# Kernel optimization log

Hardware: AMD Instinct MI355X
Metric: run time of the kernel (lower is better)

The kernel has to match this reference:

```python
import jax, jax.numpy as jnp
import numpy as np

B, S, E, H, V, L = 64, 128, 512, 1024, 32000, 1


def setup_inputs() -> dict:
    key = jax.random.key(0)
    ks = jax.random.split(key, 12)
    def rn(k, shape, scale=0.02):
        return jax.random.normal(k, shape, dtype=jnp.float32) * scale
    return dict(
        emb=rn(ks[0], (B, E), 1.0),
        hidden=rn(ks[1], (L, B, H), 1.0),
        encoder_outputs=rn(ks[2], (S, B, H), 1.0),
        z=rn(ks[3], (B, H), 1.0),
        # Attn('concat'): W_a [H, 2H], bias, scoring vector v [H]
        Wa=rn(ks[4], (H, 2 * H)), ba=jnp.zeros((H,), jnp.float32),
        v=rn(ks[5], (H,)),
        # CustomGRUCell: input/hidden/context/latent-z to 3*H gate projections
        Wx=rn(ks[6], (3 * H, E)), bx=jnp.zeros((3 * H,), jnp.float32),
        Wh=rn(ks[7], (3 * H, H)), bh=jnp.zeros((3 * H,), jnp.float32),
        Wc=rn(ks[8], (3 * H, H)), bc=jnp.zeros((3 * H,), jnp.float32),
        Wz=rn(ks[9], (3 * H, H)), bz=jnp.zeros((3 * H,), jnp.float32),
        # rnn2out: Linear(H, V)
        Wout=rn(ks[10], (V, H)), bout=jnp.zeros((V,), jnp.float32),
    )


def reference(emb, hidden, encoder_outputs, z, Wa, ba, v,
              Wx, bx, Wh, bh, Wc, bc, Wz, bz, Wout, bout):
    h_last = hidden[-1]                                              # [B,H]
    # Bahdanau 'concat' attention: score = v . tanh(Wa @ [h; enc] + ba)
    hS = jnp.broadcast_to(h_last[None], encoder_outputs.shape)       # [S,B,H]
    energy = jnp.tanh(jnp.concatenate([hS, encoder_outputs], axis=-1) @ Wa.T + ba)  # [S,B,H]
    scores = jnp.einsum('sbh,h->bs', energy, v)                      # [B,S]
    attn_weights = jax.nn.softmax(scores, axis=-1)[:, None, :]       # [B,1,S]
    enc_bt = jnp.transpose(encoder_outputs, (1, 0, 2))               # [B,S,H]
    context = jnp.einsum('bos,bsh->bh', attn_weights, enc_bt)        # [B,H]
    # Custom GRU cell: gates get extra context and latent-z additive terms
    gx = emb @ Wx.T + bx                                             # [B,3H]
    gh = h_last @ Wh.T + bh
    gc = context @ Wc.T + bc
    gz = z @ Wz.T + bz
    xr, xu, xn = jnp.split(gx + gc + gz, 3, axis=-1)
    hr, hu, hn = jnp.split(gh, 3, axis=-1)
    r = jax.nn.sigmoid(xr + hr)                                      # reset gate
    u = jax.nn.sigmoid(xu + hu)                                      # update gate
    n = jnp.tanh(xn + r * hn)                                        # candidate
    h_new = (1.0 - u) * n + u * h_last                               # [B,H]
    out = h_new @ Wout.T + bout                                      # [B,V] logits
    return out, h_new[None], attn_weights
```

## Files before the change

### kernel.cpp

```cpp
#include <hip/hip_runtime.h>
#include <hip/hip_bf16.h>
#include <math.h>

#define B_  64
#define S_  128
#define E_  512
#define H_  1024
#define V_  32000
#define H3_ 3072
#define NT_ 16

typedef __attribute__((ext_vector_type(8))) short bf16x8;
typedef __attribute__((ext_vector_type(4))) float f32x4;

__device__ __forceinline__ unsigned short f2b(float f) {
    unsigned int u = __builtin_bit_cast(unsigned int, f);
    u = (u + 0x7fffu + ((u >> 16) & 1u)) >> 16;
    return (unsigned short)u;
}

__device__ __forceinline__ void tile_acc(const float* __restrict__ A, int lda,
                                         const float* __restrict__ Wrow0, int ldw,
                                         int kspan, int t, float c[4][4],
                                         float (*As)[64], float (*Ws)[64]) {
    const int tx = t & 15, ty = t >> 4;
    const int lm = t >> 2;
    const int lk = (t & 3) * 4;
    for (int k0 = 0; k0 < kspan; k0 += 16) {
        float4 av = *(const float4*)&A[lm * lda + k0 + lk];
        float4 wv = *(const float4*)&Wrow0[(size_t)lm * ldw + k0 + lk];
        As[lk + 0][lm] = av.x; As[lk + 1][lm] = av.y;
        As[lk + 2][lm] = av.z; As[lk + 3][lm] = av.w;
        Ws[lk + 0][lm] = wv.x; Ws[lk + 1][lm] = wv.y;
        Ws[lk + 2][lm] = wv.z; Ws[lk + 3][lm] = wv.w;
        __syncthreads();
        #pragma unroll
        for (int k = 0; k < 16; ++k) {
            float4 a = *(const float4*)&As[k][ty * 4];
            float4 w = *(const float4*)&Ws[k][tx * 4];
            c[0][0] += a.x * w.x; c[0][1] += a.x * w.y; c[0][2] += a.x * w.z; c[0][3] += a.x * w.w;
            c[1][0] += a.y * w.x; c[1][1] += a.y * w.y; c[1][2] += a.y * w.z; c[1][3] += a.y * w.w;
            c[2][0] += a.z * w.x; c[2][1] += a.z * w.y; c[2][2] += a.z * w.z; c[2][3] += a.z * w.w;
            c[3][0] += a.w * w.x; c[3][1] += a.w * w.y; c[3][2] += a.w * w.z; c[3][3] += a.w * w.w;
        }
        __syncthreads();
    }
}

__device__ __forceinline__ void hproj_body(int bx, int by, const float* __restrict__ h,
                                           const float* __restrict__ Wa, float* __restrict__ hpp,
                                           int t, float (*As)[64], float (*Ws)[64]) {
    const int n0 = bx * 64;
    const int kb = by * 128;
    const int tx = t & 15, ty = t >> 4;
    float c[4][4];
    #pragma unroll
    for (int i = 0; i < 4; ++i)
        #pragma unroll
        for (int j = 0; j < 4; ++j) c[i][j] = 0.f;
    tile_acc(&h[kb], H_, &Wa[(size_t)n0 * (2 * H_) + kb], 2 * H_, 128, t, c, As, Ws);
    float* dst = hpp + (size_t)by * B_ * H_;
    #pragma unroll
    for (int i = 0; i < 4; ++i) {
        const int m = ty * 4 + i;
        #pragma unroll
        for (int j = 0; j < 4; ++j)
            dst[m * H_ + n0 + tx * 4 + j] = c[i][j];
    }
}

__global__ __launch_bounds__(256) void prologue(
    const float* __restrict__ enc, const float* __restrict__ Wa,
    const float* __restrict__ h, unsigned short* __restrict__ encb,
    unsigned short* __restrict__ wa2b, float* __restrict__ hpp) {
    __shared__ float As[16][64];
    __shared__ float Ws[16][64];
    const int bid = blockIdx.x;
    const int t = threadIdx.x;
    if (bid < 4096) {
        const size_t i8 = ((size_t)bid * 256 + t) * 8;
        float4 a = *(const float4*)&enc[i8];
        float4 b = *(const float4*)&enc[i8 + 4];
        unsigned short o[8] = { f2b(a.x), f2b(a.y), f2b(a.z), f2b(a.w),
                                f2b(b.x), f2b(b.y), f2b(b.z), f2b(b.w) };
        *(uint4*)&encb[i8] = *(uint4*)o;
    } else if (bid < 4608) {
        const int id = (bid - 4096) * 256 + t;
        const int n = id >> 7;
        const int kk = (id & 127) * 8;
        const float* src = &Wa[(size_t)n * (2 * H_) + H_ + kk];
        float4 a = *(const float4*)src;
        float4 b = *(const float4*)(src + 4);
        unsigned short o[8] = { f2b(a.x), f2b(a.y), f2b(a.z), f2b(a.w),
                                f2b(b.x), f2b(b.y), f2b(b.z), f2b(b.w) };
        *(uint4*)&wa2b[(size_t)n * H_ + kk] = *(uint4*)o;
    } else {
        const int id = bid - 4608;
        hproj_body(id & 15, id >> 4, h, Wa, hpp, t, As, Ws);
    }
}

__global__ void hproj_splitk(const float* __restrict__ h, const float* __restrict__ Wa,
                             float* __restrict__ hpp) {
    __shared__ float As[16][64];
    __shared__ float Ws[16][64];
    hproj_body(blockIdx.x, blockIdx.y, h, Wa, hpp, threadIdx.x, As, Ws);
}

__global__ void reduce_hproj(const float* __restrict__ hpp, const float* __restrict__ ba,
                             float* __restrict__ hproj) {
    const int idx = blockIdx.x * 256 + threadIdx.x;
    const int hh = idx & 1023;
    float s = ba[hh];
    #pragma unroll
    for (int c = 0; c < 8; ++c) s += hpp[(size_t)c * B_ * H_ + idx];
    hproj[idx] = s;
}

__global__ __launch_bounds__(256) void energy_mfma(
    const unsigned short* __restrict__ Ab, const unsigned short* __restrict__ Bb,
    const float* __restrict__ hproj, const float* __restrict__ v,
    float* __restrict__ partials) {
    __shared__ unsigned short As[128 * 32];
    __shared__ unsigned short Bs[128 * 32];
    const int nb = blockIdx.x;
    const int mb = blockIdx.y;
    const int m0 = mb * 128, n0 = nb * 128;
    const int t = threadIdx.x;
    const int lane = t & 63, w = t >> 6;
    const int wr = w >> 1, wc = w & 1;

    f32x4 acc[4][4];
    #pragma unroll
    for (int i = 0; i < 4; ++i)
        #pragma unroll
        for (int j = 0; j < 4; ++j) acc[i][j] = (f32x4){0.f, 0.f, 0.f, 0.f};

    for (int k0 = 0; k0 < H_; k0 += 32) {
        #pragma unroll
        for (int r = 0; r < 2; ++r) {
            const int c = r * 256 + t;
            const int row = c >> 2, slot = c & 3;
            const int sw = slot ^ ((row >> 1) & 3);
            uint4 da = *(const uint4*)&Ab[(size_t)(m0 + row) * H_ + k0 + slot * 8];
            *(uint4*)((char*)As + row * 64 + sw * 16) = da;
            uint4 db = *(const uint4*)&Bb[(size_t)(n0 + row) * H_ + k0 + slot * 8];
            *(uint4*)((char*)Bs + row * 64 + sw * 16) = db;
        }
        __syncthreads();
        bf16x8 a[4], b[4];
        #pragma unroll
        for (int i = 0; i < 4; ++i) {
            const int row = wr * 64 + i * 16 + (lane & 15);
            const int sw = (lane >> 4) ^ ((row >> 1) & 3);
            a[i] = *(const bf16x8*)((const char*)As + row * 64 + sw * 16);
        }
        #pragma unroll
        for (int j = 0; j < 4; ++j) {
            const int row = wc * 64 + j * 16 + (lane & 15);
            const int sw = (lane >> 4) ^ ((row >> 1) & 3);
            b[j] = *(const bf16x8*)((const char*)Bs + row * 64 + sw * 16);
        }
        #pragma unroll
        for (int i = 0; i < 4; ++i)
            #pragma unroll
            for (int j = 0; j < 4; ++j)
                acc[i][j] = __builtin_amdgcn_mfma_f32_16x16x32_bf16(a[i], b[j], acc[i][j], 0, 0, 0);
        __syncthreads();
    }

    float vj[4];
    #pragma unroll
    for (int j = 0; j < 4; ++j) vj[j] = v[n0 + wc * 64 + j * 16 + (lane & 15)];

    const int s = mb * 2 + wr;
    #pragma unroll
    for (int i = 0; i < 4; ++i) {
        #pragma unroll
        for (int q = 0; q < 4; ++q) {
            const int b = i * 16 + (lane >> 4) * 4 + q;
            float sum = 0.f;
            #pragma unroll
            for (int j = 0; j < 4; ++j) {
                const int n = n0 + wc * 64 + j * 16 + (lane & 15);
                sum += vj[j] * tanhf(acc[i][j][q] + hproj[b * H_ + n]);
            }
            sum += __shfl_xor(sum, 1);
            sum += __shfl_xor(sum, 2);
            sum += __shfl_xor(sum, 4);
            sum += __shfl_xor(sum, 8);
            if ((lane & 15) == 0)
                partials[((size_t)b * S_ + s) * NT_ + nb * 2 + wc] = sum;
        }
    }
}

__global__ void energy_scores(const float* __restrict__ enc, const float* __restrict__ Wa,
                              const float* __restrict__ hproj, const float* __restrict__ v,
                              float* __restrict__ partials) {
    __shared__ float As[16][64];
    __shared__ float Ws[16][64];
    __shared__ float red[64][16];
    const int nt = blockIdx.x;
    const int s  = blockIdx.y;
    const int n0 = nt * 64;
    const float* Arow = enc + (size_t)s * (B_ * H_);
    const int t  = threadIdx.x;
    const int tx = t & 15, ty = t >> 4;
    float c[4][4];
    #pragma unroll
    for (int i = 0; i < 4; ++i)
        #pragma unroll
        for (int j = 0; j < 4; ++j) c[i][j] = 0.f;
    tile_acc(Arow, H_, &Wa[(size_t)n0 * (2 * H_) + H_], 2 * H_, H_, t, c, As, Ws);
    #pragma unroll
    for (int i = 0; i < 4; ++i) {
        const int b = ty * 4 + i;
        float part = 0.f;
        #pragma unroll
        for (int j = 0; j < 4; ++j) {
            const int h = n0 + tx * 4 + j;
            part += v[h] * tanhf(c[i][j] + hproj[b * H_ + h]);
        }
        red[b][tx] = part;
    }
    __syncthreads();
    if (t < 64) {
        float sum = 0.f;
        #pragma unroll
        for (int x = 0; x < 16; ++x) sum += red[t][x];
        partials[((size_t)t * S_ + s) * NT_ + nt] = sum;
    }
}

__global__ __launch_bounds__(256) void softmax_ctx(
    const float* __restrict__ spart, const float* __restrict__ enc,
    float* __restrict__ attn, float* __restrict__ ctx) {
    __shared__ float red[128];
    __shared__ float aw[128];
    const int b = blockIdx.y;
    const int t = threadIdx.x;
    if (t < 128) {
        float sc = 0.f;
        #pragma unroll
        for (int nt = 0; nt < NT_; ++nt) sc += spart[((size_t)b * S_ + t) * NT_ + nt];
        aw[t] = sc;
        red[t] = sc;
    }
    __syncthreads();
    for (int o = 64; o > 0; o >>= 1) {
        if (t < o) red[t] = fmaxf(red[t], red[t + o]);
        __syncthreads();
    }
    const float mx = red[0];
    __syncthreads();
    if (t < 128) { aw[t] = expf(aw[t] - mx); red[t] = aw[t]; }
    __syncthreads();
    for (int o = 64; o > 0; o >>= 1) {
        if (t < o) red[t] += red[t + o];
        __syncthreads();
    }
    const float inv = 1.f / red[0];
    if (t < 128) {
        aw[t] *= inv;
        if (blockIdx.x == 0) attn[b * S_ + t] = aw[t];
    }
    __syncthreads();
    const int h = blockIdx.x * 256 + t;
    float acc = 0.f;
    for (int s = 0; s < S_; ++s)
        acc += aw[s] * enc[((size_t)s * B_ + b) * H_ + h];
    ctx[b * H_ + h] = acc;
}

__global__ void gates_splitk(const float* __restrict__ emb, const float* __restrict__ z,
                             const float* __restrict__ ctx, const float* __restrict__ h,
                             const float* __restrict__ Wx, const float* __restrict__ Wz,
                             const float* __restrict__ Wc, const float* __restrict__ Wh,
                             float* __restrict__ P) {
    __shared__ float As[16][64];
    __shared__ float Ws[16][64];
    const int n0 = blockIdx.x * 64;
    const int yc = blockIdx.y;
    const int t  = threadIdx.x;
    const int tx = t & 15, ty = t >> 4;

    const float* A; const float* W; int lda, kb;
    if (yc == 0)      { A = emb; W = Wx; lda = E_; kb = 0; }
    else if (yc <= 2) { A = z;   W = Wz; lda = H_; kb = (yc - 1) * 512; }
    else if (yc <= 4) { A = ctx; W = Wc; lda = H_; kb = (yc - 3) * 512; }
    else              { A = h;   W = Wh; lda = H_; kb = (yc - 5) * 512; }

    float c[4][4];
    #pragma unroll
    for (int i = 0; i < 4; ++i)
        #pragma unroll
        for (int j = 0; j < 4; ++j) c[i][j] = 0.f;
    tile_acc(&A[kb], lda, &W[(size_t)n0 * lda + kb], lda, 512, t, c, As, Ws);
    float* dst = P + (size_t)yc * B_ * H3_;
    #pragma unroll
    for (int i = 0; i < 4; ++i) {
        const int m = ty * 4 + i;
        #pragma unroll
        for (int j = 0; j < 4; ++j)
            dst[m * H3_ + n0 + tx * 4 + j] = c[i][j];
    }
}

__global__ void gru_k(const float* __restrict__ P, const float* __restrict__ hlast,
                      const float* __restrict__ bx, const float* __restrict__ bz,
                      const float* __restrict__ bc, const float* __restrict__ bh,
                      float* __restrict__ hnew, unsigned short* __restrict__ hnewb) {
    const int idx = blockIdx.x * 256 + threadIdx.x;
    const int b = idx >> 10, h = idx & 1023;
    float x[3], hg[3];
    #pragma unroll
    for (int g = 0; g < 3; ++g) {
        const int col = g * H_ + h;
        float sx = bx[col] + bz[col] + bc[col];
        #pragma unroll
        for (int c = 0; c < 5; ++c) sx += P[((size_t)c * B_ + b) * H3_ + col];
        float sh = bh[col];
        #pragma unroll
        for (int c = 5; c < 7; ++c) sh += P[((size_t)c * B_ + b) * H3_ + col];
        x[g] = sx; hg[g] = sh;
    }
    const float r = 1.f / (1.f + expf(-(x[0] + hg[0])));
    const float u = 1.f / (1.f + expf(-(x[1] + hg[1])));
    const float n = tanhf(x[2] + r * hg[2]);
    const float val = (1.f - u) * n + u * hlast[idx];
    hnew[idx] = val;
    if (hnewb) hnewb[idx] = f2b(val);
}

__global__ __launch_bounds__(256) void wout_mfma(
    const unsigned short* __restrict__ Ab, const float* __restrict__ W,
    const float* __restrict__ bias, float* __restrict__ C) {
    __shared__ unsigned short As[64 * 64];
    __shared__ unsigned short Bs[64 * 64];
    const int n0 = blockIdx.x * 64;
    const int t = threadIdx.x;
    const int lane = t & 63, w = t >> 6;
    const int wr = w >> 1, wc = w & 1;

    f32x4 acc[2][2];
    #pragma unroll
    for (int i = 0; i < 2; ++i)
        #pragma unroll
        for (int j = 0; j < 2; ++j) acc[i][j] = (f32x4){0.f, 0.f, 0.f, 0.f};

    for (int k0 = 0; k0 < H_; k0 += 64) {
        #pragma unroll
        for (int r = 0; r < 2; ++r) {
            const int c = r * 256 + t;
            const int row = c >> 3, slot = c & 7;
            const int sw = slot ^ (row & 7);
            uint4 da = *(const uint4*)&Ab[(size_t)row * H_ + k0 + slot * 8];
            *(uint4*)((char*)As + row * 128 + sw * 16) = da;
        }
        #pragma unroll
        for (int r = 0; r < 4; ++r) {
            const int c = r * 256 + t;
            const int row = c >> 4, q4 = c & 15;
            const float4 wv = *(const float4*)&W[(size_t)(n0 + row) * H_ + k0 + q4 * 4];
            uint2 pk;
            pk.x = (unsigned int)f2b(wv.x) | ((unsigned int)f2b(wv.y) << 16);
            pk.y = (unsigned int)f2b(wv.z) | ((unsigned int)f2b(wv.w) << 16);
            const int slot = q4 >> 1, half = q4 & 1;
            const int sw = slot ^ (row & 7);
            *(uint2*)((char*)Bs + row * 128 + sw * 16 + half * 8) = pk;
        }
        __syncthreads();
        #pragma unroll
        for (int kk = 0; kk < 2; ++kk) {
            bf16x8 a[2], b[2];
            #pragma unroll
            for (int i = 0; i < 2; ++i) {
                const int row = wr * 32 + i * 16 + (lane & 15);
                const int sw = (kk * 4 + (lane >> 4)) ^ (row & 7);
                a[i] = *(const bf16x8*)((const char*)As + row * 128 + sw * 16);
            }
            #pragma unroll
            for (int j = 0; j < 2; ++j) {
                const int row = wc * 32 + j * 16 + (lane & 15);
                const int sw = (kk * 4 + (lane >> 4)) ^ (row & 7);
                b[j] = *(const bf16x8*)((const char*)Bs + row * 128 + sw * 16);
            }
            #pragma unroll
            for (int i = 0; i < 2; ++i)
                #pragma unroll
                for (int j = 0; j < 2; ++j)
                    acc[i][j] = __builtin_amdgcn_mfma_f32_16x16x32_bf16(a[i], b[j], acc[i][j], 0, 0, 0);
        }
        __syncthreads();
    }

    #pragma unroll
    for (int i = 0; i < 2; ++i)
        #pragma unroll
        for (int j = 0; j < 2; ++j) {
            const int n = n0 + wc * 32 + j * 16 + (lane & 15);
            const float bn = bias[n];
            #pragma unroll
            for (int q = 0; q < 4; ++q) {
                const int m = wr * 32 + i * 16 + (lane >> 4) * 4 + q;
                C[(size_t)m * V_ + n] = acc[i][j][q] + bn;
            }
        }
}

__global__ void gemm_nt(const float* __restrict__ A, const float* __restrict__ W,
                        const float* __restrict__ bias, float* __restrict__ C,
                        int N, int K) {
    __shared__ float As[16][64];
    __shared__ float Ws[16][64];
    const int n0 = blockIdx.x * 64;
    const int t  = threadIdx.x;
    const int tx = t & 15, ty = t >> 4;
    float c[4][4];
    #pragma unroll
    for (int i = 0; i < 4; ++i)
        #pragma unroll
        for (int j = 0; j < 4; ++j) c[i][j] = 0.f;
    tile_acc(A, K, &W[(size_t)n0 * K], K, K, t, c, As, Ws);
    #pragma unroll
    for (int i = 0; i < 4; ++i) {
        const int m = ty * 4 + i;
        #pragma unroll
        for (int j = 0; j < 4; ++j) {
            const int n = n0 + tx * 4 + j;
            C[m * N + n] = c[i][j] + bias[n];
        }
    }
}

extern "C" void kernel_launch(void* const* d_in, const int* in_sizes, int n_in,
                              void* d_out, int out_size, void* d_ws, size_t ws_size,
                              hipStream_t stream) {
    const float* emb   = (const float*)d_in[0];
    const float* hid   = (const float*)d_in[1];
    const float* enc   = (const float*)d_in[2];
    const float* z     = (const float*)d_in[3];
    const float* Wa    = (const float*)d_in[4];
    const float* ba    = (const float*)d_in[5];
    const float* v     = (const float*)d_in[6];
    const float* Wx    = (const float*)d_in[7];
    const float* bx    = (const float*)d_in[8];
    const float* Wh    = (const float*)d_in[9];
    const float* bh    = (const float*)d_in[10];
    const float* Wc    = (const float*)d_in[11];
    const float* bc    = (const float*)d_in[12];
    const float* Wz    = (const float*)d_in[13];
    const float* bz    = (const float*)d_in[14];
    const float* Wout  = (const float*)d_in[15];
    const float* bout  = (const float*)d_in[16];

    float* out  = (float*)d_out;
    float* hnew = out + (size_t)B_ * V_;
    float* attn = hnew + (size_t)B_ * H_;

    float* hproj = (float*)d_ws;
    float* spart = hproj + (size_t)B_ * H_;
    float* ctx   = spart + (size_t)B_ * S_ * NT_;
    float* hpp   = ctx + (size_t)B_ * H_;
    float* uni   = hpp + (size_t)8 * B_ * H_;
    unsigned short* encb = (unsigned short*)uni;
    unsigned short* wa2b = encb + (size_t)S_ * B_ * H_;
    float* P = uni;
    unsigned short* hnewb = (unsigned short*)(P + (size_t)7 * B_ * H3_);
    const size_t need = (size_t)((char*)(wa2b + (size_t)H_ * H_) - (char*)d_ws);

    const float* hlast = hid;
    dim3 blk(256);

    const bool fast = (ws_size >= need);
    if (fast) {
        prologue<<<dim3(4736), blk, 0, stream>>>(enc, Wa, hlast, encb, wa2b, hpp);
        reduce_hproj<<<dim3((B_ * H_) / 256), blk, 0, stream>>>(hpp, ba, hproj);
        energy_mfma<<<dim3(H_ / 128, (S_ * B_) / 128), blk, 0, stream>>>(encb, wa2b, hproj, v, spart);
    } else {
        hproj_splitk<<<dim3(H_ / 64, 8), blk, 0, stream>>>(hlast, Wa, hpp);
        reduce_hproj<<<dim3((B_ * H_) / 256), blk, 0, stream>>>(hpp, ba, hproj);
        energy_scores<<<dim3(NT_, S_), blk, 0, stream>>>(enc, Wa, hproj, v, spart);
    }

    softmax_ctx<<<dim3(H_ / 256, B_), blk, 0, stream>>>(spart, enc, attn, ctx);

    gates_splitk<<<dim3(H3_ / 64, 7), blk, 0, stream>>>(emb, z, ctx, hlast,
                                                        Wx, Wz, Wc, Wh, P);
    gru_k<<<dim3((B_ * H_) / 256), blk, 0, stream>>>(P, hlast, bx, bz, bc, bh,
                                                     hnew, fast ? hnewb : nullptr);

    if (fast) {
        wout_mfma<<<dim3(V_ / 64), blk, 0, stream>>>(hnewb, Wout, bout, out);
    } else {
        gemm_nt<<<dim3(V_ / 64), blk, 0, stream>>>(hnew, Wout, bout, out, V_, H_);
    }
}
```

Baseline: 142.0 us.

## Fold context-independent gate GEMMs into prologue and widen energy K-tile to 64

The emb, z and h gate projections do not depend on the attention context, so they now run as extra blocks of the prologue kernel. Only the two context split-K chunks remain in a separate gates_ctx launch after softmax. This takes work off the serial critical path and lets it overlap with the bf16 conversion blocks. The energy MFMA kernel also doubles its K step to 64 with an 8-slot XOR swizzle, halving the number of barriers per tile at the cost of more shared memory. The workspace is re-laid out so P no longer aliases encb and wa2b, which raises the workspace requirement.

```diff
diff --git a/kernel.cpp b/kernel.cpp
--- a/kernel.cpp
+++ b/kernel.cpp
@@ -69,10 +69,43 @@
     }
 }
 
+__device__ __forceinline__ void gate_body(int n0, int sel,
+                                          const float* __restrict__ emb, const float* __restrict__ z,
+                                          const float* __restrict__ h,
+                                          const float* __restrict__ Wx, const float* __restrict__ Wz,
+                                          const float* __restrict__ Wh, float* __restrict__ P,
+                                          int t, float (*As)[64], float (*Ws)[64]) {
+    const int tx = t & 15, ty = t >> 4;
+    const float* A; const float* W; int lda, kb, chunk;
+    if (sel == 0)      { A = emb; W = Wx; lda = E_; kb = 0;   chunk = 0; }
+    else if (sel == 1) { A = z;   W = Wz; lda = H_; kb = 0;   chunk = 1; }
+    else if (sel == 2) { A = z;   W = Wz; lda = H_; kb = 512; chunk = 2; }
+    else if (sel == 3) { A = h;   W = Wh; lda = H_; kb = 0;   chunk = 5; }
+    else               { A = h;   W = Wh; lda = H_; kb = 512; chunk = 6; }
+    float c[4][4];
+    #pragma unroll
+    for (int i = 0; i < 4; ++i)
+        #pragma unroll
+        for (int j = 0; j < 4; ++j) c[i][j] = 0.f;
+    tile_acc(&A[kb], lda, &W[(size_t)n0 * lda + kb], lda, 512, t, c, As, Ws);
+    float* dst = P + (size_t)chunk * B_ * H3_;
+    #pragma unroll
+    for (int i = 0; i < 4; ++i) {
+        const int m = ty * 4 + i;
+        #pragma unroll
+        for (int j = 0; j < 4; ++j)
+            dst[m * H3_ + n0 + tx * 4 + j] = c[i][j];
+    }
+}
+
 __global__ __launch_bounds__(256) void prologue(
     const float* __restrict__ enc, const float* __restrict__ Wa,
-    const float* __restrict__ h, unsigned short* __restrict__ encb,
-    unsigned short* __restrict__ wa2b, float* __restrict__ hpp) {
+    const float* __restrict__ h, const float* __restrict__ emb,
+    const float* __restrict__ z,
+    const float* __restrict__ Wx, const float* __restrict__ Wz,
+    const float* __restrict__ Wh,
+    unsigned short* __restrict__ encb, unsigned short* __restrict__ wa2b,
+    float* __restrict__ hpp, float* __restrict__ P) {
     __shared__ float As[16][64];
     __shared__ float Ws[16][64];
     const int bid = blockIdx.x;
@@ -94,9 +127,12 @@
         unsigned short o[8] = { f2b(a.x), f2b(a.y), f2b(a.z), f2b(a.w),
                                 f2b(b.x), f2b(b.y), f2b(b.z), f2b(b.w) };
         *(uint4*)&wa2b[(size_t)n * H_ + kk] = *(uint4*)o;
-    } else {
+    } else if (bid < 4736) {
         const int id = bid - 4608;
         hproj_body(id & 15, id >> 4, h, Wa, hpp, t, As, Ws);
+    } else {
+        const int id = bid - 4736;
+        gate_body((id % 48) * 64, id / 48, emb, z, h, Wx, Wz, Wh, P, t, As, Ws);
     }
 }
 
@@ -121,8 +157,8 @@
     const unsigned short* __restrict__ Ab, const unsigned short* __restrict__ Bb,
     const float* __restrict__ hproj, const float* __restrict__ v,
     float* __restrict__ partials) {
-    __shared__ unsigned short As[128 * 32];
-    __shared__ unsigned short Bs[128 * 32];
+    __shared__ unsigned short As[128 * 64];
+    __shared__ unsigned short Bs[128 * 64];
     const int nb = blockIdx.x;
     const int mb = blockIdx.y;
     const int m0 = mb * 128, n0 = nb * 128;
@@ -136,36 +172,39 @@
         #pragma unroll
         for (int j = 0; j < 4; ++j) acc[i][j] = (f32x4){0.f, 0.f, 0.f, 0.f};
 
-    for (int k0 = 0; k0 < H_; k0 += 32) {
-        #pragma unroll
-        for (int r = 0; r < 2; ++r) {
+    for (int k0 = 0; k0 < H_; k0 += 64) {
+        #pragma unroll
+        for (int r = 0; r < 4; ++r) {
             const int c = r * 256 + t;
-            const int row = c >> 2, slot = c & 3;
-            const int sw = slot ^ ((row >> 1) & 3);
+            const int row = c >> 3, slot = c & 7;
+            const int sw = slot ^ (row & 7);
             uint4 da = *(const uint4*)&Ab[(size_t)(m0 + row) * H_ + k0 + slot * 8];
-            *(uint4*)((char*)As + row * 64 + sw * 16) = da;
+            *(uint4*)((char*)As + row * 128 + sw * 16) = da;
             uint4 db = *(const uint4*)&Bb[(size_t)(n0 + row) * H_ + k0 + slot * 8];
-            *(uint4*)((char*)Bs + row * 64 + sw * 16) = db;
-        }
-        __syncthreads();
-        bf16x8 a[4], b[4];
-        #pragma unroll
-        for (int i = 0; i < 4; ++i) {
-            const int row = wr * 64 + i * 16 + (lane & 15);
-            const int sw = (lane >> 4) ^ ((row >> 1) & 3);
-            a[i] = *(const bf16x8*)((const char*)As + row * 64 + sw * 16);
-        }
-        #pragma unroll
-        for (int j = 0; j < 4; ++j) {
-            const int row = wc * 64 + j * 16 + (lane & 15);
-            const int sw = (lane >> 4) ^ ((row >> 1) & 3);
-            b[j] = *(const bf16x8*)((const char*)Bs + row * 64 + sw * 16);
-        }
-        #pragma unroll
-        for (int i = 0; i < 4; ++i)
-            #pragma unroll
-            for (int j = 0; j < 4; ++j)
-                acc[i][j] = __builtin_amdgcn_mfma_f32_16x16x32_bf16(a[i], b[j], acc[i][j], 0, 0, 0);
+            *(uint4*)((char*)Bs + row * 128 + sw * 16) = db;
+        }
+        __syncthreads();
+        #pragma unroll
+        for (int kk = 0; kk < 2; ++kk) {
+            bf16x8 a[4], b[4];
+            #pragma unroll
+            for (int i = 0; i < 4; ++i) {
+                const int row = wr * 64 + i * 16 + (lane & 15);
+                const int sw = (kk * 4 + (lane >> 4)) ^ (row & 7);
+                a[i] = *(const bf16x8*)((const char*)As + row * 128 + sw * 16);
+            }
+            #pragma unroll
+            for (int j = 0; j < 4; ++j) {
+                const int row = wc * 64 + j * 16 + (lane & 15);
+                const int sw = (kk * 4 + (lane >> 4)) ^ (row & 7);
+                b[j] = *(const bf16x8*)((const char*)Bs + row * 128 + sw * 16);
+            }
+            #pragma unroll
+            for (int i = 0; i < 4; ++i)
+                #pragma unroll
+                for (int j = 0; j < 4; ++j)
+                    acc[i][j] = __builtin_amdgcn_mfma_f32_16x16x32_bf16(a[i], b[j], acc[i][j], 0, 0, 0);
+        }
         __syncthreads();
     }
 
@@ -273,6 +312,30 @@
     ctx[b * H_ + h] = acc;
 }
 
+__global__ void gates_ctx(const float* __restrict__ ctx, const float* __restrict__ Wc,
+                          float* __restrict__ P) {
+    __shared__ float As[16][64];
+    __shared__ float Ws[16][64];
+    const int n0 = blockIdx.x * 64;
+    const int kb = blockIdx.y * 512;
+    const int t  = threadIdx.x;
+    const int tx = t & 15, ty = t >> 4;
+    float c[4][4];
+    #pragma unroll
+    for (int i = 0; i < 4; ++i)
+        #pragma unroll
+        for (int j = 0; j < 4; ++j) c[i][j] = 0.f;
+    tile_acc(&ctx[kb], H_, &Wc[(size_t)n0 * H_ + kb], H_, 512, t, c, As, Ws);
+    float* dst = P + (size_t)(3 + blockIdx.y) * B_ * H3_;
+    #pragma unroll
+    for (int i = 0; i < 4; ++i) {
+        const int m = ty * 4 + i;
+        #pragma unroll
+        for (int j = 0; j < 4; ++j)
+            dst[m * H3_ + n0 + tx * 4 + j] = c[i][j];
+    }
+}
+
 __global__ void gates_splitk(const float* __restrict__ emb, const float* __restrict__ z,
                              const float* __restrict__ ctx, const float* __restrict__ h,
                              const float* __restrict__ Wx, const float* __restrict__ Wz,
@@ -284,13 +347,11 @@
     const int yc = blockIdx.y;
     const int t  = threadIdx.x;
     const int tx = t & 15, ty = t >> 4;
-
     const float* A; const float* W; int lda, kb;
     if (yc == 0)      { A = emb; W = Wx; lda = E_; kb = 0; }
     else if (yc <= 2) { A = z;   W = Wz; lda = H_; kb = (yc - 1) * 512; }
     else if (yc <= 4) { A = ctx; W = Wc; lda = H_; kb = (yc - 3) * 512; }
     else              { A = h;   W = Wh; lda = H_; kb = (yc - 5) * 512; }
-
     float c[4][4];
     #pragma unroll
     for (int i = 0; i < 4; ++i)
@@ -463,11 +524,11 @@
     float* spart = hproj + (size_t)B_ * H_;
     float* ctx   = spart + (size_t)B_ * S_ * NT_;
     float* hpp   = ctx + (size_t)B_ * H_;
-    float* uni   = hpp + (size_t)8 * B_ * H_;
-    unsigned short* encb = (unsigned short*)uni;
-    unsigned short* wa2b = encb + (size_t)S_ * B_ * H_;
-    float* P = uni;
-    unsigned short* hnewb = (unsigned short*)(P + (size_t)7 * B_ * H3_);
+    float* P     = hpp + (size_t)8 * B_ * H_;
+    float* fend  = P + (size_t)7 * B_ * H3_;
+    unsigned short* hnewb = (unsigned short*)fend;
+    unsigned short* encb  = hnewb + (size_t)B_ * H_;
+    unsigned short* wa2b  = encb + (size_t)S_ * B_ * H_;
     const size_t need = (size_t)((char*)(wa2b + (size_t)H_ * H_) - (char*)d_ws);
 
     const float* hlast = hid;
@@ -475,25 +536,22 @@
 
     const bool fast = (ws_size >= need);
     if (fast) {
-        prologue<<<dim3(4736), blk, 0, stream>>>(enc, Wa, hlast, encb, wa2b, hpp);
+        prologue<<<dim3(4976), blk, 0, stream>>>(enc, Wa, hlast, emb, z,
+                                                 Wx, Wz, Wh, encb, wa2b, hpp, P);
         reduce_hproj<<<dim3((B_ * H_) / 256), blk, 0, stream>>>(hpp, ba, hproj);
         energy_mfma<<<dim3(H_ / 128, (S_ * B_) / 128), blk, 0, stream>>>(encb, wa2b, hproj, v, spart);
+        softmax_ctx<<<dim3(H_ / 256, B_), blk, 0, stream>>>(spart, enc, attn, ctx);
+        gates_ctx<<<dim3(H3_ / 64, 2), blk, 0, stream>>>(ctx, Wc, P);
+        gru_k<<<dim3((B_ * H_) / 256), blk, 0, stream>>>(P, hlast, bx, bz, bc, bh, hnew, hnewb);
+        wout_mfma<<<dim3(V_ / 64), blk, 0, stream>>>(hnewb, Wout, bout, out);
     } else {
         hproj_splitk<<<dim3(H_ / 64, 8), blk, 0, stream>>>(hlast, Wa, hpp);
         reduce_hproj<<<dim3((B_ * H_) / 256), blk, 0, stream>>>(hpp, ba, hproj);
         energy_scores<<<dim3(NT_, S_), blk, 0, stream>>>(enc, Wa, hproj, v, spart);
-    }
-
-    softmax_ctx<<<dim3(H_ / 256, B_), blk, 0, stream>>>(spart, enc, attn, ctx);
-
-    gates_splitk<<<dim3(H3_ / 64, 7), blk, 0, stream>>>(emb, z, ctx, hlast,
-                                                        Wx, Wz, Wc, Wh, P);
-    gru_k<<<dim3((B_ * H_) / 256), blk, 0, stream>>>(P, hlast, bx, bz, bc, bh,
-                                                     hnew, fast ? hnewb : nullptr);
-
-    if (fast) {
-        wout_mfma<<<dim3(V_ / 64), blk, 0, stream>>>(hnewb, Wout, bout, out);
-    } else {
+        softmax_ctx<<<dim3(H_ / 256, B_), blk, 0, stream>>>(spart, enc, attn, ctx);
+        gates_splitk<<<dim3(H3_ / 64, 7), blk, 0, stream>>>(emb, z, ctx, hlast,
+                                                            Wx, Wz, Wc, Wh, P);
+        gru_k<<<dim3((B_ * H_) / 256), blk, 0, stream>>>(P, hlast, bx, bz, bc, bh, hnew, nullptr);
         gemm_nt<<<dim3(V_ / 64), blk, 0, stream>>>(hnew, Wout, bout, out, V_, H_);
     }
 }
```

Result: slower. 178.8 us (+25.9%).

## Deepen split-K for gates, prefetch tile loads, widen energy MFMA K-step

Applied to the files above, without the earlier changes.

The gates GEMM now splits K into 256-wide chunks across 14 blocks in y instead of 7, so more blocks run in parallel. gru_k sums the extra partials. tile_acc prefetches the next global tile into registers while computing on the current shared-memory tile, which hides load latency. energy_mfma now stages a K-slab of 64 with an 8-way XOR swizzle, halving barriers per K. The workspace layout is reordered so the larger partial buffer and the bf16 buffers do not overlap, at the cost of more workspace and more partial-sum traffic.

```diff
diff --git a/kernel.cpp b/kernel.cpp
--- a/kernel.cpp
+++ b/kernel.cpp
@@ -9,6 +9,7 @@
 #define V_  32000
 #define H3_ 3072
 #define NT_ 16
+#define NGC 14
 
 typedef __attribute__((ext_vector_type(8))) short bf16x8;
 typedef __attribute__((ext_vector_type(4))) float f32x4;
@@ -26,14 +27,18 @@
     const int tx = t & 15, ty = t >> 4;
     const int lm = t >> 2;
     const int lk = (t & 3) * 4;
+    float4 av = *(const float4*)&A[lm * lda + lk];
+    float4 wv = *(const float4*)&Wrow0[(size_t)lm * ldw + lk];
     for (int k0 = 0; k0 < kspan; k0 += 16) {
-        float4 av = *(const float4*)&A[lm * lda + k0 + lk];
-        float4 wv = *(const float4*)&Wrow0[(size_t)lm * ldw + k0 + lk];
         As[lk + 0][lm] = av.x; As[lk + 1][lm] = av.y;
         As[lk + 2][lm] = av.z; As[lk + 3][lm] = av.w;
         Ws[lk + 0][lm] = wv.x; Ws[lk + 1][lm] = wv.y;
         Ws[lk + 2][lm] = wv.z; Ws[lk + 3][lm] = wv.w;
         __syncthreads();
+        if (k0 + 16 < kspan) {
+            av = *(const float4*)&A[lm * lda + k0 + 16 + lk];
+            wv = *(const float4*)&Wrow0[(size_t)lm * ldw + k0 + 16 + lk];
+        }
         #pragma unroll
         for (int k = 0; k < 16; ++k) {
             float4 a = *(const float4*)&As[k][ty * 4];
@@ -121,8 +126,8 @@
     const unsigned short* __restrict__ Ab, const unsigned short* __restrict__ Bb,
     const float* __restrict__ hproj, const float* __restrict__ v,
     float* __restrict__ partials) {
-    __shared__ unsigned short As[128 * 32];
-    __shared__ unsigned short Bs[128 * 32];
+    __shared__ unsigned short As[128 * 64];
+    __shared__ unsigned short Bs[128 * 64];
     const int nb = blockIdx.x;
     const int mb = blockIdx.y;
     const int m0 = mb * 128, n0 = nb * 128;
@@ -136,36 +141,39 @@
         #pragma unroll
         for (int j = 0; j < 4; ++j) acc[i][j] = (f32x4){0.f, 0.f, 0.f, 0.f};
 
-    for (int k0 = 0; k0 < H_; k0 += 32) {
-        #pragma unroll
-        for (int r = 0; r < 2; ++r) {
+    for (int k0 = 0; k0 < H_; k0 += 64) {
+        #pragma unroll
+        for (int r = 0; r < 4; ++r) {
             const int c = r * 256 + t;
-            const int row = c >> 2, slot = c & 3;
-            const int sw = slot ^ ((row >> 1) & 3);
+            const int row = c >> 3, slot = c & 7;
+            const int sw = slot ^ (row & 7);
             uint4 da = *(const uint4*)&Ab[(size_t)(m0 + row) * H_ + k0 + slot * 8];
-            *(uint4*)((char*)As + row * 64 + sw * 16) = da;
+            *(uint4*)((char*)As + row * 128 + sw * 16) = da;
             uint4 db = *(const uint4*)&Bb[(size_t)(n0 + row) * H_ + k0 + slot * 8];
-            *(uint4*)((char*)Bs + row * 64 + sw * 16) = db;
-        }
-        __syncthreads();
-        bf16x8 a[4], b[4];
-        #pragma unroll
-        for (int i = 0; i < 4; ++i) {
-            const int row = wr * 64 + i * 16 + (lane & 15);
-            const int sw = (lane >> 4) ^ ((row >> 1) & 3);
-            a[i] = *(const bf16x8*)((const char*)As + row * 64 + sw * 16);
-        }
-        #pragma unroll
-        for (int j = 0; j < 4; ++j) {
-            const int row = wc * 64 + j * 16 + (lane & 15);
-            const int sw = (lane >> 4) ^ ((row >> 1) & 3);
-            b[j] = *(const bf16x8*)((const char*)Bs + row * 64 + sw * 16);
-        }
-        #pragma unroll
-        for (int i = 0; i < 4; ++i)
-            #pragma unroll
-            for (int j = 0; j < 4; ++j)
-                acc[i][j] = __builtin_amdgcn_mfma_f32_16x16x32_bf16(a[i], b[j], acc[i][j], 0, 0, 0);
+            *(uint4*)((char*)Bs + row * 128 + sw * 16) = db;
+        }
+        __syncthreads();
+        #pragma unroll
+        for (int kk = 0; kk < 2; ++kk) {
+            bf16x8 a[4], b[4];
+            #pragma unroll
+            for (int i = 0; i < 4; ++i) {
+                const int row = wr * 64 + i * 16 + (lane & 15);
+                const int sw = (kk * 4 + (lane >> 4)) ^ (row & 7);
+                a[i] = *(const bf16x8*)((const char*)As + row * 128 + sw * 16);
+            }
+            #pragma unroll
+            for (int j = 0; j < 4; ++j) {
+                const int row = wc * 64 + j * 16 + (lane & 15);
+                const int sw = (kk * 4 + (lane >> 4)) ^ (row & 7);
+                b[j] = *(const bf16x8*)((const char*)Bs + row * 128 + sw * 16);
+            }
+            #pragma unroll
+            for (int i = 0; i < 4; ++i)
+                #pragma unroll
+                for (int j = 0; j < 4; ++j)
+                    acc[i][j] = __builtin_amdgcn_mfma_f32_16x16x32_bf16(a[i], b[j], acc[i][j], 0, 0, 0);
+        }
         __syncthreads();
     }
 
@@ -284,19 +292,17 @@
     const int yc = blockIdx.y;
     const int t  = threadIdx.x;
     const int tx = t & 15, ty = t >> 4;
-
     const float* A; const float* W; int lda, kb;
-    if (yc == 0)      { A = emb; W = Wx; lda = E_; kb = 0; }
-    else if (yc <= 2) { A = z;   W = Wz; lda = H_; kb = (yc - 1) * 512; }
-    else if (yc <= 4) { A = ctx; W = Wc; lda = H_; kb = (yc - 3) * 512; }
-    else              { A = h;   W = Wh; lda = H_; kb = (yc - 5) * 512; }
-
+    if (yc < 2)       { A = emb; W = Wx; lda = E_; kb = yc * 256; }
+    else if (yc < 6)  { A = z;   W = Wz; lda = H_; kb = (yc - 2) * 256; }
+    else if (yc < 10) { A = ctx; W = Wc; lda = H_; kb = (yc - 6) * 256; }
+    else              { A = h;   W = Wh; lda = H_; kb = (yc - 10) * 256; }
     float c[4][4];
     #pragma unroll
     for (int i = 0; i < 4; ++i)
         #pragma unroll
         for (int j = 0; j < 4; ++j) c[i][j] = 0.f;
-    tile_acc(&A[kb], lda, &W[(size_t)n0 * lda + kb], lda, 512, t, c, As, Ws);
+    tile_acc(&A[kb], lda, &W[(size_t)n0 * lda + kb], lda, 256, t, c, As, Ws);
     float* dst = P + (size_t)yc * B_ * H3_;
     #pragma unroll
     for (int i = 0; i < 4; ++i) {
@@ -319,10 +325,10 @@
         const int col = g * H_ + h;
         float sx = bx[col] + bz[col] + bc[col];
         #pragma unroll
-        for (int c = 0; c < 5; ++c) sx += P[((size_t)c * B_ + b) * H3_ + col];
+        for (int c = 0; c < 10; ++c) sx += P[((size_t)c * B_ + b) * H3_ + col];
         float sh = bh[col];
         #pragma unroll
-        for (int c = 5; c < 7; ++c) sh += P[((size_t)c * B_ + b) * H3_ + col];
+        for (int c = 10; c < 14; ++c) sh += P[((size_t)c * B_ + b) * H3_ + col];
         x[g] = sx; hg[g] = sh;
     }
     const float r = 1.f / (1.f + expf(-(x[0] + hg[0])));
@@ -463,11 +469,11 @@
     float* spart = hproj + (size_t)B_ * H_;
     float* ctx   = spart + (size_t)B_ * S_ * NT_;
     float* hpp   = ctx + (size_t)B_ * H_;
-    float* uni   = hpp + (size_t)8 * B_ * H_;
-    unsigned short* encb = (unsigned short*)uni;
-    unsigned short* wa2b = encb + (size_t)S_ * B_ * H_;
-    float* P = uni;
-    unsigned short* hnewb = (unsigned short*)(P + (size_t)7 * B_ * H3_);
+    float* P     = hpp + (size_t)8 * B_ * H_;
+    float* fend  = P + (size_t)NGC * B_ * H3_;
+    unsigned short* hnewb = (unsigned short*)fend;
+    unsigned short* encb  = hnewb + (size_t)B_ * H_;
+    unsigned short* wa2b  = encb + (size_t)S_ * B_ * H_;
     const size_t need = (size_t)((char*)(wa2b + (size_t)H_ * H_) - (char*)d_ws);
 
     const float* hlast = hid;
@@ -478,22 +484,19 @@
         prologue<<<dim3(4736), blk, 0, stream>>>(enc, Wa, hlast, encb, wa2b, hpp);
         reduce_hproj<<<dim3((B_ * H_) / 256), blk, 0, stream>>>(hpp, ba, hproj);
         energy_mfma<<<dim3(H_ / 128, (S_ * B_) / 128), blk, 0, stream>>>(encb, wa2b, hproj, v, spart);
+        softmax_ctx<<<dim3(H_ / 256, B_), blk, 0, stream>>>(spart, enc, attn, ctx);
+        gates_splitk<<<dim3(H3_ / 64, NGC), blk, 0, stream>>>(emb, z, ctx, hlast,
+                                                              Wx, Wz, Wc, Wh, P);
+        gru_k<<<dim3((B_ * H_) / 256), blk, 0, stream>>>(P, hlast, bx, bz, bc, bh, hnew, hnewb);
+        wout_mfma<<<dim3(V_ / 64), blk, 0, stream>>>(hnewb, Wout, bout, out);
     } else {
         hproj_splitk<<<dim3(H_ / 64, 8), blk, 0, stream>>>(hlast, Wa, hpp);
         reduce_hproj<<<dim3((B_ * H_) / 256), blk, 0, stream>>>(hpp, ba, hproj);
         energy_scores<<<dim3(NT_, S_), blk, 0, stream>>>(enc, Wa, hproj, v, spart);
-    }
-
-    softmax_ctx<<<dim3(H_ / 256, B_), blk, 0, stream>>>(spart, enc, attn, ctx);
-
-    gates_splitk<<<dim3(H3_ / 64, 7), blk, 0, stream>>>(emb, z, ctx, hlast,
-                                                        Wx, Wz, Wc, Wh, P);
-    gru_k<<<dim3((B_ * H_) / 256), blk, 0, stream>>>(P, hlast, bx, bz, bc, bh,
-                                                     hnew, fast ? hnewb : nullptr);
-
-    if (fast) {
-        wout_mfma<<<dim3(V_ / 64), blk, 0, stream>>>(hnewb, Wout, bout, out);
-    } else {
+        softmax_ctx<<<dim3(H_ / 256, B_), blk, 0, stream>>>(spart, enc, attn, ctx);
+        gates_splitk<<<dim3(H3_ / 64, NGC), blk, 0, stream>>>(emb, z, ctx, hlast,
+                                                              Wx, Wz, Wc, Wh, P);
+        gru_k<<<dim3((B_ * H_) / 256), blk, 0, stream>>>(P, hlast, bx, bz, bc, bh, hnew, nullptr);
         gemm_nt<<<dim3(V_ / 64), blk, 0, stream>>>(hnew, Wout, bout, out, V_, H_);
     }
 }
```

Result: faster. 129.6 us (-8.7%).
